# Optimization experiments

Hardware: AMD Instinct MI355X
Metric: run time of the kernel (lower is better)

Reference implementation:

```python
import jax, jax.numpy as jnp
import numpy as np

L, D, H, FF, E, K, S, B = 2, 1024, 16, 4096, 8, 2, 1024, 8
HD = D // H
EPS = 1e-5


def setup_inputs() -> dict:
    key = jax.random.key(0)
    ks = jax.random.split(key, 18)
    sc = 0.02
    inp = {
        "src": jax.random.normal(ks[0], (S, B, D), jnp.float32),
        "pos": jax.random.normal(ks[1], (S, B, D), jnp.float32),
        "qkv_w": jax.random.normal(ks[2], (L, 3 * D, D), jnp.float32) * sc,
        "qkv_b": jnp.zeros((L, 3 * D), jnp.float32),
        "out_w": jax.random.normal(ks[3], (L, D, D), jnp.float32) * sc,
        "out_b": jnp.zeros((L, D), jnp.float32),
        "ln1_w": jnp.ones((L, D), jnp.float32),
        "ln1_b": jnp.zeros((L, D), jnp.float32),
        "ln2_w": jnp.ones((L, D), jnp.float32),
        "ln2_b": jnp.zeros((L, D), jnp.float32),
        "gate_w": jax.random.normal(ks[4], (L, E, D), jnp.float32) * sc,
        "gate_b": jnp.zeros((L, E), jnp.float32),
        "w1": jax.random.normal(ks[5], (L, E, FF, D), jnp.float32) * sc,
        "b1": jnp.zeros((L, E, FF), jnp.float32),
        "w2": jax.random.normal(ks[6], (L, E, D, FF), jnp.float32) * sc,
        "b2": jnp.zeros((L, E, D), jnp.float32),
    }
    return inp


def _ln(x, w, b):
    m = x.mean(-1, keepdims=True)
    v = ((x - m) ** 2).mean(-1, keepdims=True)
    return (x - m) * jax.lax.rsqrt(v + EPS) * w + b


def _attn(src, pos, qkv_w, qkv_b, out_w, out_b):
    qk_in = src + pos  # q = k = with_pos_embed(src, pos); v = src
    wq, wk, wv = qkv_w[:D], qkv_w[D:2 * D], qkv_w[2 * D:]
    bq, bk, bv = qkv_b[:D], qkv_b[D:2 * D], qkv_b[2 * D:]
    q = (qk_in @ wq.T + bq).reshape(S, B, H, HD)
    k = (qk_in @ wk.T + bk).reshape(S, B, H, HD)
    v = (src @ wv.T + bv).reshape(S, B, H, HD)
    scores = jnp.einsum("sbhd,tbhd->bhst", q, k) / jnp.sqrt(jnp.float32(HD))
    a = jax.nn.softmax(scores, axis=-1)
    o = jnp.einsum("bhst,tbhd->sbhd", a, v).reshape(S, B, D)
    return o @ out_w.T + out_b


def _moe(x, gate_w, gate_b, w1, b1, w2, b2):
    T = S * B
    xf = x.reshape(T, D)
    scores = xf @ gate_w.T + gate_b                      # [T, E]
    topv, topi = jax.lax.top_k(scores, K)                # [T, K]
    probs = jax.nn.softmax(topv, axis=-1)                # [T, K]
    # combine weight per (token, expert); experts not in top-k get 0
    cw = jnp.zeros((T, E), xf.dtype).at[jnp.arange(T)[:, None], topi].add(probs)
    out = jnp.zeros_like(xf)
    for e in range(E):  # small fixed loop over experts (structurally distinct GEMMs)
        h = jax.nn.relu(xf @ w1[e].T + b1[e])
        y = h @ w2[e].T + b2[e]
        out = out + cw[:, e:e + 1] * y
    return out.reshape(S, B, D), probs, topi


def _aux(probs, topi):
    usage = jnp.zeros(E, probs.dtype).at[topi.reshape(-1)].add(probs.reshape(-1))
    p = usage / usage.sum()
    return -(p * jnp.log(p + 1e-9)).sum()


def reference(src, pos, qkv_w, qkv_b, out_w, out_b, ln1_w, ln1_b, ln2_w, ln2_b,
              gate_w, gate_b, w1, b1, w2, b2):
    x = src
    aux = jnp.float32(0.0)
    for l in range(L):
        a = _attn(x, pos, qkv_w[l], qkv_b[l], out_w[l], out_b[l])
        x = _ln(x + a, ln1_w[l], ln1_b[l])
        m, probs, topi = _moe(x, gate_w[l], gate_b[l], w1[l], b1[l], w2[l], b2[l])
        aux = aux + (1.0 / L) * _aux(probs, topi)
        x = _ln(x + m, ln2_w[l], ln2_b[l])
    return x, aux
```

## Files before the change

kernel.cpp:

```cpp
#include <hip/hip_runtime.h>

#define L_ 2
#define D_ 1024
#define H_ 16
#define FF_ 4096
#define E_ 8
#define S_ 1024
#define B_ 8
#define T_ (S_*B_)
#define TP_ 17408
#define NBLK_MAX 136
#define HALF_BLK 68

typedef _Float16 half8 __attribute__((ext_vector_type(8)));
typedef _Float16 half4_t __attribute__((ext_vector_type(4)));
typedef float f32x4 __attribute__((ext_vector_type(4)));

__device__ __forceinline__ f32x4 mfma16(half8 a, half8 b, f32x4 c) {
  return __builtin_amdgcn_mfma_f32_16x16x32_f16(a, b, c, 0, 0, 0);
}

struct hl2 { _Float16 h, l; };
__device__ __forceinline__ hl2 split2(float v) {
  hl2 r;
  r.h = (_Float16)v;
  r.l = (_Float16)(v - (float)r.h);
  return r;
}

__device__ __forceinline__ void gll16(const _Float16* g, _Float16* l) {
  __builtin_amdgcn_global_load_lds(
      (const __attribute__((address_space(1))) unsigned int*)g,
      (__attribute__((address_space(3))) unsigned int*)l, 16, 0, 0);
}

template<int NPROD, bool GATHER, bool MOE, bool RELU, int OUT>
__global__ __launch_bounds__(256, 2)
void gemm_pl(const _Float16* __restrict__ Ah, const _Float16* __restrict__ Al,
             const float* __restrict__ B, const float* __restrict__ bias,
             float* __restrict__ C, _Float16* __restrict__ Ch,
             _Float16* __restrict__ Cl,
             int K, int N, long bExpStride, int biasExpStride,
             const int* __restrict__ gtok,
             const int* __restrict__ nblk,
             const unsigned char* __restrict__ blk_e, int mb0)
{
  const int mb = blockIdx.x, nb = blockIdx.y;
  const float* Bp = B;
  const float* biasp = bias;
  if constexpr (MOE) {
    if (mb0 + mb >= *nblk) return;
    const int e = blk_e[mb0 + mb];
    Bp += (long)e * bExpStride;
    biasp += (long)e * biasExpStride;
  }
  const int bcol = nb * 128;
  constexpr int PL = (NPROD == 3) ? 2 : 1;
  constexpr int BUFH = PL * 8192;
  constexpr int NCH = PL * 2;
  __shared__ __align__(16) _Float16 lds[2*BUFH];

  const int tid = threadIdx.x;
  const int lane = tid & 63, wid = tid >> 6;
  const int wr = wid >> 1, wc = wid & 1;
  const int fkc = lane >> 4;

  const _Float16* asrc[NCH];
  int adst[NCH];
#pragma unroll
  for (int i = 0; i < NCH; ++i) {
    const int ch = wid + i*4;
    const int pl = ch >> 3, blk = ch & 7;
    const int rowin = blk*16 + (lane & 15);
    long ar;
    if constexpr (GATHER) ar = gtok[(mb0 + mb)*128 + rowin];
    else ar = (long)mb*128 + rowin;
    asrc[i] = (pl ? Al : Ah) + ar*(long)K + ((lane >> 4) << 3);
    adst[i] = pl*4096 + blk*512;
  }
  const float* bsrc[2];
  int bdst[2];
#pragma unroll
  for (int j = 0; j < 2; ++j) {
    const int s = tid + j*256;
    const int l = s & 63;
    const int rowcol = (s >> 6)*16 + (l & 15);
    const int kh = (l >> 4) << 3;
    bsrc[j] = Bp + (long)(bcol + rowcol)*K + kh;
    bdst[j] = PL*4096 + s*8;
  }

  float4 brg[2][2];
  auto stageA = [&](int buf, int k0) {
#pragma unroll
    for (int i = 0; i < NCH; ++i) gll16(asrc[i] + k0, lds + buf + adst[i]);
  };
  auto loadB = [&](int k0) {
#pragma unroll
    for (int j = 0; j < 2; ++j) {
      brg[j][0] = *(const float4*)(bsrc[j] + k0);
      brg[j][1] = *(const float4*)(bsrc[j] + k0 + 4);
    }
  };
  auto writeB = [&](int buf) {
#pragma unroll
    for (int j = 0; j < 2; ++j) {
      half8 hh; half8 ll;
      { hl2 s = split2(brg[j][0].x); hh[0]=s.h; ll[0]=s.l; }
      { hl2 s = split2(brg[j][0].y); hh[1]=s.h; ll[1]=s.l; }
      { hl2 s = split2(brg[j][0].z); hh[2]=s.h; ll[2]=s.l; }
      { hl2 s = split2(brg[j][0].w); hh[3]=s.h; ll[3]=s.l; }
      { hl2 s = split2(brg[j][1].x); hh[4]=s.h; ll[4]=s.l; }
      { hl2 s = split2(brg[j][1].y); hh[5]=s.h; ll[5]=s.l; }
      { hl2 s = split2(brg[j][1].z); hh[6]=s.h; ll[6]=s.l; }
      { hl2 s = split2(brg[j][1].w); hh[7]=s.h; ll[7]=s.l; }
      *(half8*)&lds[buf + bdst[j]] = hh;
      if constexpr (NPROD == 3) *(half8*)&lds[buf + bdst[j] + 4096] = ll;
    }
  };

  f32x4 acc[4][4];
#pragma unroll
  for (int m = 0; m < 4; ++m)
#pragma unroll
    for (int n = 0; n < 4; ++n) acc[m][n] = (f32x4){0.f, 0.f, 0.f, 0.f};

  const int NT = K / 32;
  stageA(0, 0);
  loadB(0);
  writeB(0);
  __syncthreads();

  for (int t = 0; t < NT; ++t) {
    const int cur = (t & 1) * BUFH;
    const int nxt = ((t + 1) & 1) * BUFH;
    if (t + 1 < NT) { stageA(nxt, (t+1)*32); loadB((t+1)*32); }
    half8 ahf[4], bhf[4], alf[4], blf[4];
#pragma unroll
    for (int m = 0; m < 4; ++m) {
      ahf[m] = *(const half8*)&lds[cur + (wr*4 + m)*512 + lane*8];
      if constexpr (NPROD == 3) alf[m] = *(const half8*)&lds[cur + 4096 + (wr*4 + m)*512 + lane*8];
      bhf[m] = *(const half8*)&lds[cur + PL*4096 + (wc*4 + m)*512 + lane*8];
      if constexpr (NPROD == 3) blf[m] = *(const half8*)&lds[cur + PL*4096 + 4096 + (wc*4 + m)*512 + lane*8];
    }
#pragma unroll
    for (int m = 0; m < 4; ++m)
#pragma unroll
      for (int n = 0; n < 4; ++n) {
        if constexpr (NPROD == 3) {
          acc[m][n] = mfma16(alf[m], bhf[n], acc[m][n]);
          acc[m][n] = mfma16(ahf[m], blf[n], acc[m][n]);
        }
        acc[m][n] = mfma16(ahf[m], bhf[n], acc[m][n]);
      }
    if (t + 1 < NT) writeB(nxt);
    __syncthreads();
  }

  int cbase;
  if constexpr (MOE) cbase = (OUT != 0) ? mb*128 : (mb0 + mb)*128;
  else cbase = mb*128;
  const int fr = lane & 15;
  const int r0 = fkc * 4;
#pragma unroll
  for (int m = 0; m < 4; ++m) {
    const int grow = cbase + wr*64 + m*16 + r0;
#pragma unroll
    for (int n = 0; n < 4; ++n) {
      const int gcol = bcol + wc*64 + n*16 + fr;
      const float bv = biasp[gcol];
#pragma unroll
      for (int r = 0; r < 4; ++r) {
        float v = acc[m][n][r] + bv;
        if constexpr (RELU) v = fmaxf(v, 0.f);
        const long idx = (long)(grow + r) * N + gcol;
        if constexpr (OUT == 0) {
          C[idx] = v;
        } else {
          hl2 s = split2(v);
          Ch[idx] = s.h;
          if constexpr (OUT == 1) Cl[idx] = s.l;
        }
      }
    }
  }
}

__global__ __launch_bounds__(256) void addpos_kernel(const float* __restrict__ x,
    const float* __restrict__ p,
    _Float16* __restrict__ XPh, _Float16* __restrict__ XPl,
    _Float16* __restrict__ XFh, _Float16* __restrict__ XFl)
{
  const long i = (long)blockIdx.x * 256 + threadIdx.x;
  const float4 a = ((const float4*)x)[i];
  const float4 b = ((const float4*)p)[i];
  half4_t fh, fl, ph, pl;
  { hl2 s = split2(a.x); fh[0]=s.h; fl[0]=s.l; }
  { hl2 s = split2(a.y); fh[1]=s.h; fl[1]=s.l; }
  { hl2 s = split2(a.z); fh[2]=s.h; fl[2]=s.l; }
  { hl2 s = split2(a.w); fh[3]=s.h; fl[3]=s.l; }
  { hl2 s = split2(a.x+b.x); ph[0]=s.h; pl[0]=s.l; }
  { hl2 s = split2(a.y+b.y); ph[1]=s.h; pl[1]=s.l; }
  { hl2 s = split2(a.z+b.z); ph[2]=s.h; pl[2]=s.l; }
  { hl2 s = split2(a.w+b.w); ph[3]=s.h; pl[3]=s.l; }
  *(half4_t*)&XFh[i*4] = fh; *(half4_t*)&XFl[i*4] = fl;
  *(half4_t*)&XPh[i*4] = ph; *(half4_t*)&XPl[i*4] = pl;
}

__global__ __launch_bounds__(256) void vtrans_kernel(
    const _Float16* __restrict__ Vh, const _Float16* __restrict__ Vl,
    _Float16* __restrict__ Vth, _Float16* __restrict__ Vtl)
{
  const int st = blockIdx.x, bh = blockIdx.y;
  const int b = bh >> 4, h = bh & 15;
  __shared__ __align__(16) _Float16 th[64*64];
  __shared__ __align__(16) _Float16 tl[64*64];
  const int tid = threadIdx.x;
#pragma unroll
  for (int i = 0; i < 2; ++i) {
    const int r = i*32 + (tid >> 3);
    const int c = tid & 7;
    const long t = (long)(st*64 + r)*8 + b;
    const long ga = t*1024 + h*64 + c*8;
    const int la = r*64 + ((c ^ (r & 7)) << 3);
    *(half8*)&th[la] = *(const half8*)&Vh[ga];
    *(half8*)&tl[la] = *(const half8*)&Vl[ga];
  }
  __syncthreads();
#pragma unroll
  for (int i = 0; i < 2; ++i) {
    const int d = i*32 + (tid >> 3);
    const int sc = tid & 7;
    half8 oh, ol;
#pragma unroll
    for (int j = 0; j < 8; ++j) {
      const int s = sc*8 + j;
      const int la = s*64 + (((d >> 3) ^ (s & 7)) << 3) + (d & 7);
      oh[j] = th[la]; ol[j] = tl[la];
    }
    const long oa = ((long)bh*64 + d)*1024 + st*64 + sc*8;
    *(half8*)&Vth[oa] = oh;
    *(half8*)&Vtl[oa] = ol;
  }
}

__global__ __launch_bounds__(256, 4) void attn_kernel(
    const _Float16* __restrict__ QKh, const _Float16* __restrict__ QKl,
    const _Float16* __restrict__ Vth, const _Float16* __restrict__ Vtl,
    _Float16* __restrict__ Oh, _Float16* __restrict__ Ol)
{
  const int qb = blockIdx.x;
  const int bh = blockIdx.y;
  const int b = bh >> 4, h = bh & 15;
  const int tid = threadIdx.x, lane = tid & 63, wid = tid >> 6;
  const int fr = lane & 15, fkc = lane >> 4;
  __shared__ __align__(16) _Float16 Kh_s[32*64];
  __shared__ __align__(16) _Float16 Kl_s[32*64];
  __shared__ __align__(16) _Float16 Ph[4][16*32];
  __shared__ __align__(16) _Float16 Pl[4][16*32];

  half8 qfh[2], qfl[2];
  {
    const long qbase = ((long)(qb*64 + wid*16 + fr)*8 + b)*2048 + h*64;
#pragma unroll
    for (int dc = 0; dc < 2; ++dc) {
      qfh[dc] = *(const half8*)&QKh[qbase + dc*32 + fkc*8];
      qfl[dc] = *(const half8*)&QKl[qbase + dc*32 + fkc*8];
    }
  }
  f32x4 oacc[4];
#pragma unroll
  for (int c = 0; c < 4; ++c) oacc[c] = (f32x4){0.f,0.f,0.f,0.f};
  float lsum[4] = {0.f,0.f,0.f,0.f};

  for (int kt = 0; kt < 32; ++kt) {
    __syncthreads();
#pragma unroll
    for (int ch = wid; ch < 8; ch += 4) {
      const int pl = ch >> 2, qt = ch & 3;
      const int r = qt*8 + (lane >> 3), c = lane & 7;
      const long t = (long)(kt*32 + r)*8 + b;
      const _Float16* srcp = (pl ? QKl : QKh) + t*2048 + 1024 + h*64 + ((c ^ (r & 7)) << 3);
      _Float16* dstp = (pl ? Kl_s : Kh_s) + (qt << 9);
      gll16(srcp, dstp);
    }
    __syncthreads();

    f32x4 st[2];
    st[0] = (f32x4){0.f,0.f,0.f,0.f}; st[1] = (f32x4){0.f,0.f,0.f,0.f};
#pragma unroll
    for (int tc = 0; tc < 2; ++tc)
#pragma unroll
      for (int dc = 0; dc < 2; ++dc) {
        const int kr = tc*16 + fr;
        const int cc = ((dc*4 + fkc) ^ (kr & 7)) << 3;
        const half8 kfh = *(const half8*)&Kh_s[kr*64 + cc];
        const half8 kfl = *(const half8*)&Kl_s[kr*64 + cc];
        st[tc] = mfma16(qfl[dc], kfh, st[tc]);
        st[tc] = mfma16(qfh[dc], kfl, st[tc]);
        st[tc] = mfma16(qfh[dc], kfh, st[tc]);
      }

    float p0[4], p1[4];
#pragma unroll
    for (int r = 0; r < 4; ++r) {
      p0[r] = __expf(st[0][r] * 0.125f);
      p1[r] = __expf(st[1][r] * 0.125f);
      lsum[r] += p0[r] + p1[r];
    }

#pragma unroll
    for (int r = 0; r < 4; ++r) {
      const int prow = fkc*4 + r;
      hl2 s0 = split2(p0[r]);
      hl2 s1 = split2(p1[r]);
      const int i0 = prow*32 + (((fr>>3) ^ (prow&3)) << 3) + (fr & 7);
      const int c1 = fr + 16;
      const int i1 = prow*32 + (((c1>>3) ^ (prow&3)) << 3) + (c1 & 7);
      Ph[wid][i0] = s0.h;  Pl[wid][i0] = s0.l;
      Ph[wid][i1] = s1.h;  Pl[wid][i1] = s1.l;
    }
    const int ip = fr*32 + ((fkc ^ (fr&3)) << 3);
    const half8 pfh = *(const half8*)&Ph[wid][ip];
    const half8 pfl = *(const half8*)&Pl[wid][ip];

    const long vtb = ((long)bh*64)*1024 + kt*32 + fkc*8;
#pragma unroll
    for (int c = 0; c < 4; ++c) {
      const long va = vtb + (long)(c*16 + fr)*1024;
      const half8 vfh = *(const half8*)&Vth[va];
      const half8 vfl = *(const half8*)&Vtl[va];
      oacc[c] = mfma16(pfl, vfh, oacc[c]);
      oacc[c] = mfma16(pfh, vfl, oacc[c]);
      oacc[c] = mfma16(pfh, vfh, oacc[c]);
    }
  }
#pragma unroll
  for (int r = 0; r < 4; ++r) {
    float l = lsum[r];
    l += __shfl_xor(l, 1); l += __shfl_xor(l, 2);
    l += __shfl_xor(l, 4); l += __shfl_xor(l, 8);
    lsum[r] = l;
  }
#pragma unroll
  for (int c = 0; c < 4; ++c)
#pragma unroll
    for (int r = 0; r < 4; ++r) {
      const int srow = qb*64 + wid*16 + fkc*4 + r;
      const long idx = ((long)srow * B_ + b) * 1024 + h*64 + c*16 + fr;
      hl2 s = split2(oacc[c][r] / lsum[r]);
      Oh[idx] = s.h; Ol[idx] = s.l;
    }
}

template<bool PLANES>
__global__ __launch_bounds__(256) void ln_kernel(
    const float* __restrict__ a, const float* __restrict__ b,
    const float* __restrict__ w, const float* __restrict__ bias,
    float* __restrict__ out, _Float16* __restrict__ Lh, _Float16* __restrict__ Ll)
{
  const int row = blockIdx.x, tid = threadIdx.x;
  const long base = (long)row * D_;
  const float4 va = *(const float4*)&a[base + tid*4];
  const float4 vb = *(const float4*)&b[base + tid*4];
  const float x0 = va.x+vb.x, x1 = va.y+vb.y, x2 = va.z+vb.z, x3 = va.w+vb.w;
  float s = (x0+x1)+(x2+x3);
  float q = (x0*x0+x1*x1)+(x2*x2+x3*x3);
  for (int m = 1; m < 64; m <<= 1) { s += __shfl_xor(s, m); q += __shfl_xor(q, m); }
  __shared__ float rs[4], rq[4];
  const int wid = tid >> 6;
  if ((tid & 63) == 0) { rs[wid] = s; rq[wid] = q; }
  __syncthreads();
  s = (rs[0]+rs[1])+(rs[2]+rs[3]);
  q = (rq[0]+rq[1])+(rq[2]+rq[3]);
  const float mean = s * (1.f/D_);
  const float var = q * (1.f/D_) - mean*mean;
  const float inv = rsqrtf(var + 1e-5f);
  const float4 vw = *(const float4*)&w[tid*4];
  const float4 vbi = *(const float4*)&bias[tid*4];
  float4 r;
  r.x = (x0-mean)*inv*vw.x + vbi.x;
  r.y = (x1-mean)*inv*vw.y + vbi.y;
  r.z = (x2-mean)*inv*vw.z + vbi.z;
  r.w = (x3-mean)*inv*vw.w + vbi.w;
  *(float4*)&out[base + tid*4] = r;
  if constexpr (PLANES) {
    half4_t hh, ll;
    { hl2 t = split2(r.x); hh[0]=t.h; ll[0]=t.l; }
    { hl2 t = split2(r.y); hh[1]=t.h; ll[1]=t.l; }
    { hl2 t = split2(r.z); hh[2]=t.h; ll[2]=t.l; }
    { hl2 t = split2(r.w); hh[3]=t.h; ll[3]=t.l; }
    *(half4_t*)&Lh[base + tid*4] = hh;
    *(half4_t*)&Ll[base + tid*4] = ll;
  }
}

__global__ __launch_bounds__(256) void gate_kernel(const float* __restrict__ x,
    const float* __restrict__ gw, const float* __restrict__ gb, float* __restrict__ sc)
{
  const int t = blockIdx.x * 32 + (threadIdx.x >> 3);
  const int e = threadIdx.x & 7;
  const float* xr = x + (long)t * D_;
  const float* wr = gw + (long)e * D_;
  float a0 = 0, a1 = 0, a2 = 0, a3 = 0;
  for (int d = 0; d < D_; d += 4) {
    const float4 av = *(const float4*)&xr[d];
    const float4 wv = *(const float4*)&wr[d];
    a0 += av.x*wv.x; a1 += av.y*wv.y; a2 += av.z*wv.z; a3 += av.w*wv.w;
  }
  sc[t*E_ + e] = (a0+a1)+(a2+a3) + gb[e];
}

__global__ __launch_bounds__(256) void topk_kernel(const float* __restrict__ sc,
    int* __restrict__ topi, float* __restrict__ tkwt, int* __restrict__ cnt)
{
  const int t = blockIdx.x * 256 + threadIdx.x;
  const float* r = sc + (long)t * E_;
  float v1 = -1e30f, v2 = -1e30f; int i1 = 0, i2 = 0;
#pragma unroll
  for (int e = 0; e < E_; ++e) {
    const float v = r[e];
    if (v > v1) { v2 = v1; i2 = i1; v1 = v; i1 = e; }
    else if (v > v2) { v2 = v; i2 = e; }
  }
  const float e2 = expf(v2 - v1);
  const float inv = 1.f / (1.f + e2);
  topi[t*2] = i1; topi[t*2+1] = i2;
  tkwt[t*2] = inv; tkwt[t*2+1] = e2 * inv;
  atomicAdd(&cnt[i1], 1); atomicAdd(&cnt[i2], 1);
}

__global__ void plan_kernel(const int* __restrict__ cnt, int* __restrict__ cursor,
    int* __restrict__ nblk, unsigned char* __restrict__ blk_e, int* __restrict__ pairs_tok)
{
  __shared__ int soff[9];
  __shared__ int scnt[8];
  if (threadIdx.x == 0) {
    int o = 0;
#pragma unroll
    for (int e = 0; e < E_; ++e) {
      soff[e] = o; cursor[e] = o; scnt[e] = cnt[e];
      o += (cnt[e] + 127) & ~127;
    }
    soff[8] = o;
    *nblk = o >> 7;
  }
  __syncthreads();
  const int total = soff[8];
  for (int bidx = threadIdx.x; bidx < (total >> 7); bidx += 256) {
    const int rb = bidx << 7;
    int e = 0;
    while (e < 7 && rb >= soff[e+1]) ++e;
    blk_e[bidx] = (unsigned char)e;
  }
#pragma unroll
  for (int e = 0; e < E_; ++e) {
    const int s0 = soff[e] + scnt[e], s1 = soff[e+1];
    for (int i = s0 + (int)threadIdx.x; i < s1; i += 256) pairs_tok[i] = 0;
  }
}

__global__ __launch_bounds__(256) void fill_kernel(const int* __restrict__ topi,
    int* __restrict__ cursor, int* __restrict__ pairs_tok, int* __restrict__ tkpos)
{
  const int t = blockIdx.x * 256 + threadIdx.x;
#pragma unroll
  for (int k = 0; k < 2; ++k) {
    const int e = topi[t*2+k];
    const int pos = atomicAdd(&cursor[e], 1);
    pairs_tok[pos] = t;
    tkpos[t*2+k] = pos;
  }
}

__global__ __launch_bounds__(256) void combine_kernel(const float* __restrict__ y,
    const int* __restrict__ tkpos, const float* __restrict__ tkwt, float* __restrict__ out)
{
  const int t = blockIdx.x, d = threadIdx.x * 4;
  const long p0 = tkpos[t*2], p1 = tkpos[t*2+1];
  const float w0 = tkwt[t*2], w1 = tkwt[t*2+1];
  const float4 a = *(const float4*)&y[p0*D_ + d];
  const float4 b = *(const float4*)&y[p1*D_ + d];
  float4 r;
  r.x = w0*a.x + w1*b.x; r.y = w0*a.y + w1*b.y;
  r.z = w0*a.z + w1*b.z; r.w = w0*a.w + w1*b.w;
  *(float4*)&out[(long)t*D_ + d] = r;
}

__global__ void aux_kernel(const int* __restrict__ topi, const float* __restrict__ tkwt,
    float* __restrict__ aux_out, int first)
{
  float u[8] = {0,0,0,0,0,0,0,0};
  for (int i = threadIdx.x; i < T_*2; i += 256) {
    const int e = topi[i]; const float wv = tkwt[i];
#pragma unroll
    for (int k = 0; k < 8; ++k) u[k] += (e == k) ? wv : 0.f;
  }
  __shared__ float red[256];
  float usage[8];
#pragma unroll
  for (int e = 0; e < 8; ++e) {
    red[threadIdx.x] = u[e];
    __syncthreads();
    for (int s = 128; s > 0; s >>= 1) {
      if ((int)threadIdx.x < s) red[threadIdx.x] += red[threadIdx.x + s];
      __syncthreads();
    }
    usage[e] = red[0];
    __syncthreads();
  }
  if (threadIdx.x == 0) {
    float sum = 0;
#pragma unroll
    for (int e = 0; e < 8; ++e) sum += usage[e];
    float Hh = 0;
#pragma unroll
    for (int e = 0; e < 8; ++e) {
      const float p = usage[e] / sum;
      Hh -= p * logf(p + 1e-9f);
    }
    if (first) *aux_out = 0.5f * Hh;
    else *aux_out += 0.5f * Hh;
  }
}

extern "C" void kernel_launch(void* const* d_in, const int* in_sizes, int n_in,
                              void* d_out, int out_size, void* d_ws, size_t ws_size,
                              hipStream_t stream) {
  const float* src    = (const float*)d_in[0];
  const float* pos    = (const float*)d_in[1];
  const float* qkv_w  = (const float*)d_in[2];
  const float* qkv_b  = (const float*)d_in[3];
  const float* out_w  = (const float*)d_in[4];
  const float* out_b  = (const float*)d_in[5];
  const float* ln1_w  = (const float*)d_in[6];
  const float* ln1_b  = (const float*)d_in[7];
  const float* ln2_w  = (const float*)d_in[8];
  const float* ln2_b  = (const float*)d_in[9];
  const float* gate_w = (const float*)d_in[10];
  const float* gate_b = (const float*)d_in[11];
  const float* w1     = (const float*)d_in[12];
  const float* b1     = (const float*)d_in[13];
  const float* w2     = (const float*)d_in[14];
  const float* b2     = (const float*)d_in[15];
  float* out = (float*)d_out;

  char* ws = (char*)d_ws;
  size_t off = 0;
  auto alloc = [&](size_t bytes) -> char* {
    char* p = ws + off;
    off = (off + bytes + 255) & ~(size_t)255;
    return p;
  };
  const size_t TD = (size_t)T_ * D_;
  float* x_master = (float*)alloc(TD*4);
  float* ln1_f    = (float*)alloc(TD*4);
  float* moe_out  = (float*)alloc(TD*4);
  _Float16* L1h   = (_Float16*)alloc(TD*2);
  _Float16* L1l   = (_Float16*)alloc(TD*2);
  float* scores   = (float*)alloc((size_t)T_*E_*4);
  int*   topi     = (int*)alloc((size_t)T_*2*4);
  float* tkwt     = (float*)alloc((size_t)T_*2*4);
  int*   tkpos    = (int*)alloc((size_t)T_*2*4);
  int*   pairs_tok= (int*)alloc((size_t)TP_*4);
  int*   cnt      = (int*)alloc(E_*4);
  int*   cursor   = (int*)alloc(E_*4);
  int*   nblk     = (int*)alloc(256);
  unsigned char* blk_e = (unsigned char*)alloc(256);
  const size_t attn_sz = TD*24;
  const size_t hrows = (size_t)HALF_BLK * 128;
  const size_t moe_sz = hrows*FF_*2*2 + (size_t)TP_*D_*4;
  char* uni = alloc(attn_sz > moe_sz ? attn_sz : moe_sz);
  _Float16* QKh = (_Float16*)uni;
  _Float16* QKl = (_Float16*)(uni + TD*4);
  _Float16* Vh  = (_Float16*)(uni + TD*8);
  _Float16* Vl  = (_Float16*)(uni + TD*10);
  _Float16* Vth = (_Float16*)(uni + TD*12);
  _Float16* Vtl = (_Float16*)(uni + TD*14);
  _Float16* XPh = (_Float16*)(uni + TD*16);
  _Float16* XPl = (_Float16*)(uni + TD*18);
  _Float16* XFh = (_Float16*)(uni + TD*20);
  _Float16* XFl = (_Float16*)(uni + TD*22);
  _Float16* Oh  = XFh;
  _Float16* Ol  = XFl;
  _Float16* Hh  = (_Float16*)uni;
  _Float16* Hl  = (_Float16*)(uni + hrows*FF_*2);
  float* y_buf  = (float*)(uni + hrows*FF_*4);

  for (int l = 0; l < L_; ++l) {
    const float* x_f  = (l == 0) ? src : x_master;
    const float* qkvw = qkv_w + (size_t)l*3*D_*D_;
    const float* qkvb = qkv_b + (size_t)l*3*D_;
    const float* outw = out_w + (size_t)l*D_*D_;
    const float* outb = out_b + (size_t)l*D_;
    const float* w1l  = w1 + (size_t)l*E_*FF_*D_;
    const float* b1l  = b1 + (size_t)l*E_*FF_;
    const float* w2l  = w2 + (size_t)l*E_*D_*FF_;
    const float* b2l  = b2 + (size_t)l*E_*D_;

    addpos_kernel<<<TD/1024, 256, 0, stream>>>(x_f, pos, XPh, XPl, XFh, XFl);
    gemm_pl<3,false,false,false,1><<<dim3(T_/128, 16), 256, 0, stream>>>(
        XPh, XPl, qkvw, qkvb, nullptr, QKh, QKl,
        D_, 2*D_, 0, 0, nullptr, nullptr, nullptr, 0);
    gemm_pl<3,false,false,false,1><<<dim3(T_/128, 8), 256, 0, stream>>>(
        XFh, XFl, qkvw + (size_t)2*D_*D_, qkvb + 2*D_, nullptr, Vh, Vl,
        D_, D_, 0, 0, nullptr, nullptr, nullptr, 0);
    vtrans_kernel<<<dim3(16, 128), 256, 0, stream>>>(Vh, Vl, Vth, Vtl);
    attn_kernel<<<dim3(16, 128), 256, 0, stream>>>(QKh, QKl, Vth, Vtl, Oh, Ol);
    gemm_pl<3,false,false,false,0><<<dim3(T_/128, 8), 256, 0, stream>>>(
        Oh, Ol, outw, outb, moe_out, nullptr, nullptr,
        D_, D_, 0, 0, nullptr, nullptr, nullptr, 0);
    ln_kernel<true><<<T_, 256, 0, stream>>>(x_f, moe_out, ln1_w + (size_t)l*D_,
        ln1_b + (size_t)l*D_, ln1_f, L1h, L1l);
    gate_kernel<<<T_/32, 256, 0, stream>>>(ln1_f, gate_w + (size_t)l*E_*D_,
        gate_b + (size_t)l*E_, scores);
    (void)hipMemsetAsync(cnt, 0, E_*4, stream);
    topk_kernel<<<T_/256, 256, 0, stream>>>(scores, topi, tkwt, cnt);
    plan_kernel<<<1, 256, 0, stream>>>(cnt, cursor, nblk, blk_e, pairs_tok);
    fill_kernel<<<T_/256, 256, 0, stream>>>(topi, cursor, pairs_tok, tkpos);
    for (int half = 0; half < 2; ++half) {
      const int mb0 = half * HALF_BLK;
      if (l == 0) {
        gemm_pl<3,true,true,true,1><<<dim3(HALF_BLK, FF_/128), 256, 0, stream>>>(
            L1h, L1l, w1l, b1l, nullptr, Hh, Hl,
            D_, FF_, (long)FF_*D_, FF_, pairs_tok, nblk, blk_e, mb0);
        gemm_pl<3,false,true,false,0><<<dim3(HALF_BLK, D_/128), 256, 0, stream>>>(
            Hh, Hl, w2l, b2l, y_buf, nullptr, nullptr,
            FF_, D_, (long)D_*FF_, D_, nullptr, nblk, blk_e, mb0);
      } else {
        gemm_pl<1,true,true,true,2><<<dim3(HALF_BLK, FF_/128), 256, 0, stream>>>(
            L1h, L1l, w1l, b1l, nullptr, Hh, nullptr,
            D_, FF_, (long)FF_*D_, FF_, pairs_tok, nblk, blk_e, mb0);
        gemm_pl<1,false,true,false,0><<<dim3(HALF_BLK, D_/128), 256, 0, stream>>>(
            Hh, nullptr, w2l, b2l, y_buf, nullptr, nullptr,
            FF_, D_, (long)D_*FF_, D_, nullptr, nblk, blk_e, mb0);
      }
    }
    combine_kernel<<<T_, 256, 0, stream>>>(y_buf, tkpos, tkwt, moe_out);
    aux_kernel<<<1, 256, 0, stream>>>(topi, tkwt, out + TD, l == 0 ? 1 : 0);
    float* ln2_dst = (l == L_-1) ? out : x_master;
    ln_kernel<false><<<T_, 256, 0, stream>>>(ln1_f, moe_out, ln2_w + (size_t)l*D_,
        ln2_b + (size_t)l*D_, ln2_dst, nullptr, nullptr);
  }
}
```

Measured before the change: 4.026 ms.

## Drop LDS double buffering in GEMM and raise occupancy via launch bounds

The GEMM kernel goes from a double-buffered LDS pipeline to a single buffer. Each K-step now syncs, stages A through global_load_lds, writes the converted B tile, syncs again, then prefetches the next B slice into registers. This halves LDS use and raises launch-bounds occupancy (3 or 4 blocks per CU) so wave-level parallelism can hide latency. The cost is a second barrier per K-step and the loss of overlap between A staging and MFMA compute within a block.

After: 4.077 ms. About the same (+1.3%).

```diff
diff --git a/kernel.cpp b/kernel.cpp
--- a/kernel.cpp
+++ b/kernel.cpp
@@ -35,7 +35,7 @@
 }
 
 template<int NPROD, bool GATHER, bool MOE, bool RELU, int OUT>
-__global__ __launch_bounds__(256, 2)
+__global__ __launch_bounds__(256, NPROD == 3 ? 3 : 4)
 void gemm_pl(const _Float16* __restrict__ Ah, const _Float16* __restrict__ Al,
              const float* __restrict__ B, const float* __restrict__ bias,
              float* __restrict__ C, _Float16* __restrict__ Ch,
@@ -56,45 +56,39 @@
   }
   const int bcol = nb * 128;
   constexpr int PL = (NPROD == 3) ? 2 : 1;
-  constexpr int BUFH = PL * 8192;
-  constexpr int NCH = PL * 2;
-  __shared__ __align__(16) _Float16 lds[2*BUFH];
+  __shared__ __align__(16) _Float16 lds[PL*8192];
 
   const int tid = threadIdx.x;
   const int lane = tid & 63, wid = tid >> 6;
   const int wr = wid >> 1, wc = wid & 1;
-  const int fkc = lane >> 4;
-
-  const _Float16* asrc[NCH];
-  int adst[NCH];
-#pragma unroll
-  for (int i = 0; i < NCH; ++i) {
+
+  const _Float16* asrc[PL*2];
+  int adst[PL*2];
+#pragma unroll
+  for (int i = 0; i < PL*2; ++i) {
     const int ch = wid + i*4;
-    const int pl = ch >> 3, blk = ch & 7;
-    const int rowin = blk*16 + (lane & 15);
-    long ar;
-    if constexpr (GATHER) ar = gtok[(mb0 + mb)*128 + rowin];
-    else ar = (long)mb*128 + rowin;
-    asrc[i] = (pl ? Al : Ah) + ar*(long)K + ((lane >> 4) << 3);
-    adst[i] = pl*4096 + blk*512;
+    const int plane = ch >> 3, blk = ch & 7;
+    const int rc = blk*16 + (lane & 15);
+    const int kh = (lane >> 4) * 8;
+    long r;
+    if constexpr (GATHER) r = gtok[(mb0 + mb)*128 + rc];
+    else r = (long)mb*128 + rc;
+    asrc[i] = (plane ? Al : Ah) + r*(long)K + kh;
+    adst[i] = plane*4096 + blk*512;
   }
   const float* bsrc[2];
   int bdst[2];
 #pragma unroll
   for (int j = 0; j < 2; ++j) {
     const int s = tid + j*256;
-    const int l = s & 63;
-    const int rowcol = (s >> 6)*16 + (l & 15);
-    const int kh = (l >> 4) << 3;
-    bsrc[j] = Bp + (long)(bcol + rowcol)*K + kh;
-    bdst[j] = PL*4096 + s*8;
+    const int blk = s >> 6, l = s & 63;
+    const int rc = blk*16 + (l & 15);
+    const int kh = (l >> 4) * 8;
+    bsrc[j] = Bp + (long)(bcol + rc)*K + kh;
+    bdst[j] = PL*4096 + blk*512 + l*8;
   }
 
   float4 brg[2][2];
-  auto stageA = [&](int buf, int k0) {
-#pragma unroll
-    for (int i = 0; i < NCH; ++i) gll16(asrc[i] + k0, lds + buf + adst[i]);
-  };
   auto loadB = [&](int k0) {
 #pragma unroll
     for (int j = 0; j < 2; ++j) {
@@ -102,7 +96,7 @@
       brg[j][1] = *(const float4*)(bsrc[j] + k0 + 4);
     }
   };
-  auto writeB = [&](int buf) {
+  auto writeB = [&]() {
 #pragma unroll
     for (int j = 0; j < 2; ++j) {
       half8 hh; half8 ll;
@@ -114,8 +108,8 @@
       { hl2 s = split2(brg[j][1].y); hh[5]=s.h; ll[5]=s.l; }
       { hl2 s = split2(brg[j][1].z); hh[6]=s.h; ll[6]=s.l; }
       { hl2 s = split2(brg[j][1].w); hh[7]=s.h; ll[7]=s.l; }
-      *(half8*)&lds[buf + bdst[j]] = hh;
-      if constexpr (NPROD == 3) *(half8*)&lds[buf + bdst[j] + 4096] = ll;
+      *(half8*)&lds[bdst[j]] = hh;
+      if constexpr (NPROD == 3) *(half8*)&lds[bdst[j] + 4096] = ll;
     }
   };
 
@@ -126,22 +120,24 @@
     for (int n = 0; n < 4; ++n) acc[m][n] = (f32x4){0.f, 0.f, 0.f, 0.f};
 
   const int NT = K / 32;
-  stageA(0, 0);
   loadB(0);
-  writeB(0);
-  __syncthreads();
-
   for (int t = 0; t < NT; ++t) {
-    const int cur = (t & 1) * BUFH;
-    const int nxt = ((t + 1) & 1) * BUFH;
-    if (t + 1 < NT) { stageA(nxt, (t+1)*32); loadB((t+1)*32); }
+    const int k0 = t * 32;
+    __syncthreads();
+#pragma unroll
+    for (int i = 0; i < PL*2; ++i) gll16(asrc[i] + k0, lds + adst[i]);
+    writeB();
+    __syncthreads();
+    if (t + 1 < NT) loadB(k0 + 32);
     half8 ahf[4], bhf[4], alf[4], blf[4];
 #pragma unroll
     for (int m = 0; m < 4; ++m) {
-      ahf[m] = *(const half8*)&lds[cur + (wr*4 + m)*512 + lane*8];
-      if constexpr (NPROD == 3) alf[m] = *(const half8*)&lds[cur + 4096 + (wr*4 + m)*512 + lane*8];
-      bhf[m] = *(const half8*)&lds[cur + PL*4096 + (wc*4 + m)*512 + lane*8];
-      if constexpr (NPROD == 3) blf[m] = *(const half8*)&lds[cur + PL*4096 + 4096 + (wc*4 + m)*512 + lane*8];
+      ahf[m] = *(const half8*)&lds[(wr*4 + m)*512 + lane*8];
+      bhf[m] = *(const half8*)&lds[PL*4096 + (wc*4 + m)*512 + lane*8];
+      if constexpr (NPROD == 3) {
+        alf[m] = *(const half8*)&lds[4096 + (wr*4 + m)*512 + lane*8];
+        blf[m] = *(const half8*)&lds[PL*4096 + 4096 + (wc*4 + m)*512 + lane*8];
+      }
     }
 #pragma unroll
     for (int m = 0; m < 4; ++m)
@@ -153,15 +149,13 @@
         }
         acc[m][n] = mfma16(ahf[m], bhf[n], acc[m][n]);
       }
-    if (t + 1 < NT) writeB(nxt);
-    __syncthreads();
   }
 
   int cbase;
   if constexpr (MOE) cbase = (OUT != 0) ? mb*128 : (mb0 + mb)*128;
   else cbase = mb*128;
   const int fr = lane & 15;
-  const int r0 = fkc * 4;
+  const int r0 = (lane >> 4) * 4;
 #pragma unroll
   for (int m = 0; m < 4; ++m) {
     const int grow = cbase + wr*64 + m*16 + r0;
```
